# Performance work log

Measured on AMD Instinct MI355X. Metric: run time of the kernel, lower is better.

The kernel has to match this reference:

```python
import jax, jax.numpy as jnp
import numpy as np

N_E = 8192
E_DIM = 256
B = 32768


def setup_inputs() -> dict:
    key = jax.random.key(0)
    kz, ke = jax.random.split(key)
    z = jax.random.normal(kz, (B, E_DIM), dtype=jnp.float32)
    # matches nn.Embedding init: uniform(-1/n_e, 1/n_e)
    embedding = jax.random.uniform(ke, (N_E, E_DIM), dtype=jnp.float32,
                                   minval=-1.0 / N_E, maxval=1.0 / N_E)
    return {"z": z, "embedding": embedding}


def reference(z, embedding):
    # squared euclidean distances: [B, n_e]
    d = (jnp.sum(z * z, axis=1, keepdims=True)
         + jnp.sum(embedding * embedding, axis=1)
         - 2.0 * jnp.einsum('bd,nd->bn', z, embedding))
    min_encoding_indices = jnp.argmin(d, axis=1)          # [B] int
    z_q = embedding[min_encoding_indices]                 # [B, e_dim] gather
    return z_q, min_encoding_indices
```

## Files before the change

### kernel.cpp

```cpp
#include <hip/hip_runtime.h>

constexpr int NE = 8192;
constexpr int ED = 256;
constexpr int BS = 32768;
constexpr float DELTA = 4e-4f;

typedef short bf16x8 __attribute__((ext_vector_type(8)));
typedef float f32x4 __attribute__((ext_vector_type(4)));

constexpr size_t WSTR = (size_t)NE * 64;

__device__ __forceinline__ short f2bf(float f) {
    unsigned u = __float_as_uint(f);
    u = u + 0x7FFFu + ((u >> 16) & 1u);
    return (short)(u >> 16);
}
__device__ __forceinline__ unsigned bf16_rd(float x) {
    unsigned u = __float_as_uint(x);
    unsigned h = u >> 16;
    if ((u & 0x80000000u) && (u & 0xFFFFu)) ++h;
    return h;
}
__device__ __forceinline__ unsigned umn(unsigned a, unsigned b) { return a < b ? a : b; }
__device__ __forceinline__ unsigned umx(unsigned a, unsigned b) { return a > b ? a : b; }

__global__ void sq_np_kernel(const float* __restrict__ a, float* __restrict__ out) {
    int gtid = blockIdx.x * blockDim.x + threadIdx.x;
    int wave = gtid >> 6;
    int lane = threadIdx.x & 63;
    int sub  = lane & 7;
    int row  = wave * 8 + (lane >> 3);
    const float* p = a + (size_t)row * ED;
    float b0 = 0.f, b1 = 0.f;
#pragma unroll
    for (int t = 0; t < 16; ++t) { float v = p[8 * t + sub];       b0 = __fadd_rn(b0, __fmul_rn(v, v)); }
#pragma unroll
    for (int t = 0; t < 16; ++t) { float v = p[128 + 8 * t + sub]; b1 = __fadd_rn(b1, __fmul_rn(v, v)); }
    b0 = __fadd_rn(b0, __shfl_xor(b0, 1));
    b0 = __fadd_rn(b0, __shfl_xor(b0, 2));
    b0 = __fadd_rn(b0, __shfl_xor(b0, 4));
    b1 = __fadd_rn(b1, __shfl_xor(b1, 1));
    b1 = __fadd_rn(b1, __shfl_xor(b1, 2));
    b1 = __fadd_rn(b1, __shfl_xor(b1, 4));
    if (sub == 0) out[row] = __fadd_rn(b0, b1);
}

__global__ void cvt_ebT_kernel(const float* __restrict__ e, char* __restrict__ ebT) {
    int i = blockIdx.x * blockDim.x + threadIdx.x;
    int c = i >> 5;
    int u = i & 31;
    int w = u >> 2, lg = u & 3;
    const float* p = e + (size_t)c * ED + w * 32 + lg * 8;
    float4 v0 = *reinterpret_cast<const float4*>(p);
    float4 v1 = *reinterpret_cast<const float4*>(p + 4);
    bf16x8 h;
    h[0] = f2bf(v0.x); h[1] = f2bf(v0.y); h[2] = f2bf(v0.z); h[3] = f2bf(v0.w);
    h[4] = f2bf(v1.x); h[5] = f2bf(v1.y); h[6] = f2bf(v1.z); h[7] = f2bf(v1.w);
    *reinterpret_cast<bf16x8*>(ebT + (size_t)w * WSTR + (size_t)c * 64 + lg * 16) = h;
}

__global__ void e2slot_kernel(const float* __restrict__ e2, char* __restrict__ ebT) {
    int c = blockIdx.x * blockDim.x + threadIdx.x;
    bf16x8 h = {};
    h[0] = f2bf(e2[c] * -0.5f);
    bf16x8 zz = {};
    char* p = ebT + 8 * WSTR + (size_t)c * 64;
    *reinterpret_cast<bf16x8*>(p)      = h;
    *reinterpret_cast<bf16x8*>(p + 16) = zz;
    *reinterpret_cast<bf16x8*>(p + 32) = zz;
    *reinterpret_cast<bf16x8*>(p + 48) = zz;
}

__device__ __forceinline__ void load_step(bf16x8 (&b)[2][2], const char* abase, int S) {
    int t_ = S >> 3, s_ = S & 7;
    size_t colbyte = (size_t)((t_ << 6) + ((s_ >> 2) << 5)) << 6;
    const char* p = abase + (size_t)((s_ & 3) << 1) * WSTR + colbyte;
    b[0][0] = *reinterpret_cast<const bf16x8*>(p);
    b[0][1] = *reinterpret_cast<const bf16x8*>(p + WSTR);
    b[1][0] = *reinterpret_cast<const bf16x8*>(p + 1024);
    b[1][1] = *reinterpret_cast<const bf16x8*>(p + WSTR + 1024);
}

__global__ __launch_bounds__(256, 2) void vq_pass1(
        const float* __restrict__ z, const char* __restrict__ ebT,
        uint2* __restrict__ wsp) {
    const int tid  = threadIdx.x;
    const int wid  = tid >> 6, lane = tid & 63;
    const int l15  = lane & 15, lg = lane >> 4;
    const int kblk = blockIdx.x;
    const int rg   = (kblk & 7) | ((kblk >> 5) << 3);
    const int q    = (kblk >> 3) & 3;
    const int c0q  = q * 2048;
    const int wr0  = rg * 256 + wid * 64;

    bf16x8 zreg[4][8];
#pragma unroll
    for (int j = 0; j < 4; ++j) {
        const float* zr = z + (size_t)(wr0 + j * 16 + l15) * ED + lg * 8;
#pragma unroll
        for (int t8 = 0; t8 < 8; ++t8) {
            float4 v0 = *reinterpret_cast<const float4*>(zr + t8 * 32);
            float4 v1 = *reinterpret_cast<const float4*>(zr + t8 * 32 + 4);
            bf16x8 h;
            h[0] = f2bf(v0.x); h[1] = f2bf(v0.y); h[2] = f2bf(v0.z); h[3] = f2bf(v0.w);
            h[4] = f2bf(v1.x); h[5] = f2bf(v1.y); h[6] = f2bf(v1.z); h[7] = f2bf(v1.w);
            zreg[j][t8] = h;
        }
    }
    bf16x8 zE = {};
    if (lg == 0) zE[0] = (short)0x3F80;

    const char* abase = ebT + (size_t)(c0q + l15) * 64 + lg * 16;

    bf16x8 buf[2][2][2];
    bf16x8 bufE[2];
    load_step(buf[0], abase, 0);

    unsigned rk1[4], rk2[4];

    for (int t = 0; t < 32; ++t) {
        f32x4 acc[2][4];
#pragma unroll
        for (int s = 0; s < 8; ++s) {
            if ((s & 3) == 0) {
#pragma unroll
                for (int i2 = 0; i2 < 2; ++i2)
#pragma unroll
                    for (int j = 0; j < 4; ++j) acc[i2][j] = (f32x4){0.f, 0.f, 0.f, 0.f};
                size_t colbyte = (size_t)((t << 6) + ((s >> 2) << 5)) << 6;
                bufE[0] = *reinterpret_cast<const bf16x8*>(abase + 8 * WSTR + colbyte);
                bufE[1] = *reinterpret_cast<const bf16x8*>(abase + 8 * WSTR + colbyte + 1024);
            }
            int Sn = t * 8 + s + 1;
            Sn = Sn > 255 ? 255 : Sn;
            load_step(buf[(s + 1) & 1], abase, Sn);
#pragma unroll
            for (int tt = 0; tt < 2; ++tt)
#pragma unroll
                for (int i2 = 0; i2 < 2; ++i2)
#pragma unroll
                    for (int j = 0; j < 4; ++j)
                        acc[i2][j] = __builtin_amdgcn_mfma_f32_16x16x32_bf16(
                            buf[s & 1][i2][tt], zreg[j][(s & 3) * 2 + tt],
                            acc[i2][j], 0, 0, 0);

            if ((s & 3) == 3) {
                const int i0 = (s >> 2) * 2;
#pragma unroll
                for (int i2 = 0; i2 < 2; ++i2)
#pragma unroll
                    for (int j = 0; j < 4; ++j)
                        acc[i2][j] = __builtin_amdgcn_mfma_f32_16x16x32_bf16(
                            bufE[i2], zE, acc[i2][j], 0, 0, 0);

                const unsigned cb = (unsigned)((t & 1) * 64 + lg * 4);
#pragma unroll
                for (int j = 0; j < 4; ++j) {
                    unsigned c1 = 0xFFFFFFFFu, c2 = 0xFFFFFFFFu;
#pragma unroll
                    for (int qp = 0; qp < 2; ++qp) {
                        float va = fmaf(-2.f, acc[0][j][qp * 2],     0.5f);
                        float vb = fmaf(-2.f, acc[0][j][qp * 2 + 1], 0.5f);
                        unsigned ka = (__float_as_uint(va) & 0xFFFFFF80u) | (cb + i0 * 16 + qp * 2);
                        unsigned kb = (__float_as_uint(vb) & 0xFFFFFF80u) | (cb + i0 * 16 + qp * 2 + 1);
                        unsigned lo = umn(ka, kb), hi = umx(ka, kb);
                        unsigned mx = umx(c1, lo);
                        c1 = umn(c1, lo);
                        c2 = umn(umn(c2, hi), mx);
                        va = fmaf(-2.f, acc[1][j][qp * 2],     0.5f);
                        vb = fmaf(-2.f, acc[1][j][qp * 2 + 1], 0.5f);
                        ka = (__float_as_uint(va) & 0xFFFFFF80u) | (cb + (i0 + 1) * 16 + qp * 2);
                        kb = (__float_as_uint(vb) & 0xFFFFFF80u) | (cb + (i0 + 1) * 16 + qp * 2 + 1);
                        lo = umn(ka, kb); hi = umx(ka, kb);
                        mx = umx(c1, lo);
                        c1 = umn(c1, lo);
                        c2 = umn(umn(c2, hi), mx);
                    }
                    if (i0 == 0) {
                        if ((t & 1) == 0) { rk1[j] = c1; rk2[j] = c2; }
                        else {
                            unsigned mxh = umx(rk1[j], c1);
                            rk1[j] = umn(rk1[j], c1);
                            rk2[j] = umn(umn(rk2[j], c2), mxh);
                        }
                    } else {
                        unsigned mxh = umx(rk1[j], c1);
                        c1 = umn(rk1[j], c1);
                        c2 = umn(umn(rk2[j], c2), mxh);
                        if ((t & 1) == 0) {
                            rk1[j] = c1; rk2[j] = c2;
                        } else {
#pragma unroll
                            for (int off = 16; off < 64; off <<= 1) {
                                unsigned o1 = (unsigned)__shfl_xor((int)c1, off);
                                unsigned o2 = (unsigned)__shfl_xor((int)c2, off);
                                unsigned mx2 = umx(c1, o1);
                                c1 = umn(c1, o1);
                                c2 = umn(umn(c2, o2), mx2);
                            }
                            if (lg == 0) {
                                float m1f = __uint_as_float(c1 & 0xFFFFFF80u) - 0.5f;
                                float m2f = __uint_as_float(c2 & 0xFFFFFF80u) - 0.5f;
                                wsp[(size_t)(wr0 + j * 16 + l15) * 64 + (q * 16 + (t >> 1))] =
                                    make_uint2(__float_as_uint(m1f),
                                               (bf16_rd(m2f) << 16) | (c1 & 0x7Fu));
                            }
                        }
                    }
                }
            }
        }
    }
}

__global__ __launch_bounds__(256) void vq_pass2(
        const float* __restrict__ z, const float* __restrict__ e,
        const float* __restrict__ z2, const float* __restrict__ e2,
        const uint2* __restrict__ wsp, float* __restrict__ out) {
    __shared__ __align__(16) float zrow[4][ED];
    const int wid = threadIdx.x >> 6, lane = threadIdx.x & 63;
    const int r = blockIdx.x * 4 + wid;

    *reinterpret_cast<float4*>(&zrow[wid][lane * 4]) =
        *reinterpret_cast<const float4*>(z + (size_t)r * ED + lane * 4);
    __syncthreads();

    const float z2r = z2[r];
    uint2 p = wsp[(size_t)r * 64 + lane];
    float m1 = __uint_as_float(p.x);
    int   i8 = (int)(p.y & 0xFFu);
    float m2 = __uint_as_float(p.y & 0xFFFF0000u);

    float rmn = m1;
#pragma unroll
    for (int off = 1; off < 64; off <<= 1) rmn = fminf(rmn, __shfl_xor(rmn, off));
    const float thr = rmn + DELTA;

    const bool cF = (m2 <= thr);
    const bool cS = (m1 <= thr) && !cF;
    unsigned long long bS = __ballot(cS);
    unsigned long long bF = __ballot(cF);

    float bd = 3.4e38f;
    int   bc = NE;

    int myCol = -1;
    int cnt = 0;
    unsigned long long m = bS;
    while (true) {
        bool flush = (m == 0) || (cnt == 64);
        if (flush) {
            if (cnt > 0) {
                int ecol = (myCol >= 0) ? myCol : 0;
                const float* ec = e + (size_t)ecol * ED;
                float a0 = 0.f, a1 = 0.f, a2 = 0.f, a3 = 0.f;
#pragma unroll 8
                for (int t = 0; t < 64; ++t) {
                    float4 ev = *reinterpret_cast<const float4*>(ec + 4 * t);
                    float4 zv = *reinterpret_cast<const float4*>(&zrow[wid][4 * t]);
                    a0 = __fadd_rn(a0, __fmul_rn(zv.x, ev.x));
                    a1 = __fadd_rn(a1, __fmul_rn(zv.y, ev.y));
                    a2 = __fadd_rn(a2, __fmul_rn(zv.z, ev.z));
                    a3 = __fadd_rn(a3, __fmul_rn(zv.w, ev.w));
                }
                float s = __fadd_rn(__fadd_rn(a0, a1), __fadd_rn(a2, a3));
                float d = __fsub_rn(__fadd_rn(z2r, e2[ecol]), __fmul_rn(2.0f, s));
                if (myCol >= 0 && (d < bd || (d == bd && ecol < bc))) { bd = d; bc = ecol; }
                myCol = -1; cnt = 0;
            }
            if (m == 0) break;
        }
        int ch = __builtin_ctzll(m); m &= m - 1;
        int col = ch * 128 + __shfl(i8, ch);
        if (lane == cnt) myCol = col;
        ++cnt;
    }

    m = bF;
    while (m) {
        int ch = __builtin_ctzll(m); m &= m - 1;
#pragma unroll
        for (int hh = 0; hh < 2; ++hh) {
            int col = ch * 128 + hh * 64 + lane;
            const float* ec = e + (size_t)col * ED;
            float a0 = 0.f, a1 = 0.f, a2 = 0.f, a3 = 0.f;
#pragma unroll 8
            for (int t = 0; t < 64; ++t) {
                float4 ev = *reinterpret_cast<const float4*>(ec + 4 * t);
                float4 zv = *reinterpret_cast<const float4*>(&zrow[wid][4 * t]);
                a0 = __fadd_rn(a0, __fmul_rn(zv.x, ev.x));
                a1 = __fadd_rn(a1, __fmul_rn(zv.y, ev.y));
                a2 = __fadd_rn(a2, __fmul_rn(zv.z, ev.z));
                a3 = __fadd_rn(a3, __fmul_rn(zv.w, ev.w));
            }
            float s = __fadd_rn(__fadd_rn(a0, a1), __fadd_rn(a2, a3));
            float d = __fsub_rn(__fadd_rn(z2r, e2[col]), __fmul_rn(2.0f, s));
            if (d < bd || (d == bd && col < bc)) { bd = d; bc = col; }
        }
    }

#pragma unroll
    for (int off = 1; off < 64; off <<= 1) {
        float od = __shfl_xor(bd, off);
        int   oc = __shfl_xor(bc, off);
        if (od < bd || (od == bd && oc < bc)) { bd = od; bc = oc; }
    }
    if (lane == 0) out[(size_t)BS * ED + r] = (float)bc;
    *reinterpret_cast<float4*>(out + (size_t)r * ED + lane * 4) =
        *reinterpret_cast<const float4*>(e + (size_t)bc * ED + lane * 4);
}

extern "C" void kernel_launch(void* const* d_in, const int* in_sizes, int n_in,
                              void* d_out, int out_size, void* d_ws, size_t ws_size,
                              hipStream_t stream) {
    const float* z = (const float*)d_in[0];
    const float* e = (const float*)d_in[1];
    float* out   = (float*)d_out;
    float* e2np  = (float*)d_ws;
    float* z2np  = e2np + NE;
    uint2* wsp   = (uint2*)(z2np + BS);
    char*  ebT   = (char*)(wsp + (size_t)BS * 64);

    hipLaunchKernelGGL(sq_np_kernel, dim3(NE / 32), dim3(256), 0, stream, e, e2np);
    hipLaunchKernelGGL(sq_np_kernel, dim3(BS / 32), dim3(256), 0, stream, z, z2np);
    hipLaunchKernelGGL(cvt_ebT_kernel, dim3(NE * ED / 8 / 256), dim3(256), 0, stream, e, ebT);
    hipLaunchKernelGGL(e2slot_kernel, dim3(NE / 256), dim3(256), 0, stream, e2np, ebT);
    hipLaunchKernelGGL(vq_pass1, dim3(512), dim3(256), 0, stream, z, ebT, wsp);
    hipLaunchKernelGGL(vq_pass2, dim3(BS / 4), dim3(256), 0, stream, z, e, z2np, e2np, wsp, out);
}
```

Before: 290.1 us.

## Fold -2 scale and bias into MFMA, use med3 top-2, halve rows per wave

Pre-scales the bf16 codebook by -2 and puts e2 plus a constant 0.5 bias into the extra MFMA slot, so accumulators already hold the distance offset and the per-element fma disappears. The top-2 tracking now uses v_med3_u32 instead of min/max chains. Each wave handles 32 rows instead of 64, with twice as many blocks and three blocks per CU, trading fewer registers and more occupancy for more codebook reloads per row. The wave-row mapping and the pass2 workspace layout must stay consistent with the new row grouping.

```diff
diff --git a/kernel.cpp b/kernel.cpp
--- a/kernel.cpp
+++ b/kernel.cpp
@@ -23,6 +23,11 @@
 }
 __device__ __forceinline__ unsigned umn(unsigned a, unsigned b) { return a < b ? a : b; }
 __device__ __forceinline__ unsigned umx(unsigned a, unsigned b) { return a > b ? a : b; }
+__device__ __forceinline__ unsigned med3(unsigned a, unsigned b, unsigned c) {
+    unsigned r;
+    asm("v_med3_u32 %0, %1, %2, %3" : "=v"(r) : "v"(a), "v"(b), "v"(c));
+    return r;
+}
 
 __global__ void sq_np_kernel(const float* __restrict__ a, float* __restrict__ out) {
     int gtid = blockIdx.x * blockDim.x + threadIdx.x;
@@ -54,15 +59,18 @@
     float4 v0 = *reinterpret_cast<const float4*>(p);
     float4 v1 = *reinterpret_cast<const float4*>(p + 4);
     bf16x8 h;
-    h[0] = f2bf(v0.x); h[1] = f2bf(v0.y); h[2] = f2bf(v0.z); h[3] = f2bf(v0.w);
-    h[4] = f2bf(v1.x); h[5] = f2bf(v1.y); h[6] = f2bf(v1.z); h[7] = f2bf(v1.w);
+    h[0] = f2bf(v0.x * -2.f); h[1] = f2bf(v0.y * -2.f);
+    h[2] = f2bf(v0.z * -2.f); h[3] = f2bf(v0.w * -2.f);
+    h[4] = f2bf(v1.x * -2.f); h[5] = f2bf(v1.y * -2.f);
+    h[6] = f2bf(v1.z * -2.f); h[7] = f2bf(v1.w * -2.f);
     *reinterpret_cast<bf16x8*>(ebT + (size_t)w * WSTR + (size_t)c * 64 + lg * 16) = h;
 }
 
 __global__ void e2slot_kernel(const float* __restrict__ e2, char* __restrict__ ebT) {
     int c = blockIdx.x * blockDim.x + threadIdx.x;
     bf16x8 h = {};
-    h[0] = f2bf(e2[c] * -0.5f);
+    h[0] = f2bf(e2[c]);
+    h[1] = f2bf(0.25f);
     bf16x8 zz = {};
     char* p = ebT + 8 * WSTR + (size_t)c * 64;
     *reinterpret_cast<bf16x8*>(p)      = h;
@@ -81,7 +89,7 @@
     b[1][1] = *reinterpret_cast<const bf16x8*>(p + WSTR + 1024);
 }
 
-__global__ __launch_bounds__(256, 2) void vq_pass1(
+__global__ __launch_bounds__(256, 3) void vq_pass1(
         const float* __restrict__ z, const char* __restrict__ ebT,
         uint2* __restrict__ wsp) {
     const int tid  = threadIdx.x;
@@ -91,11 +99,11 @@
     const int rg   = (kblk & 7) | ((kblk >> 5) << 3);
     const int q    = (kblk >> 3) & 3;
     const int c0q  = q * 2048;
-    const int wr0  = rg * 256 + wid * 64;
-
-    bf16x8 zreg[4][8];
-#pragma unroll
-    for (int j = 0; j < 4; ++j) {
+    const int wr0  = rg * 128 + wid * 32;
+
+    bf16x8 zreg[2][8];
+#pragma unroll
+    for (int j = 0; j < 2; ++j) {
         const float* zr = z + (size_t)(wr0 + j * 16 + l15) * ED + lg * 8;
 #pragma unroll
         for (int t8 = 0; t8 < 8; ++t8) {
@@ -108,7 +116,7 @@
         }
     }
     bf16x8 zE = {};
-    if (lg == 0) zE[0] = (short)0x3F80;
+    if (lg == 0) { zE[0] = (short)0x3F80; zE[1] = (short)0x4000; }
 
     const char* abase = ebT + (size_t)(c0q + l15) * 64 + lg * 16;
 
@@ -116,17 +124,17 @@
     bf16x8 bufE[2];
     load_step(buf[0], abase, 0);
 
-    unsigned rk1[4], rk2[4];
+    unsigned rk1[2], rk2[2];
 
     for (int t = 0; t < 32; ++t) {
-        f32x4 acc[2][4];
+        f32x4 acc[2][2];
 #pragma unroll
         for (int s = 0; s < 8; ++s) {
             if ((s & 3) == 0) {
 #pragma unroll
                 for (int i2 = 0; i2 < 2; ++i2)
 #pragma unroll
-                    for (int j = 0; j < 4; ++j) acc[i2][j] = (f32x4){0.f, 0.f, 0.f, 0.f};
+                    for (int j = 0; j < 2; ++j) acc[i2][j] = (f32x4){0.f, 0.f, 0.f, 0.f};
                 size_t colbyte = (size_t)((t << 6) + ((s >> 2) << 5)) << 6;
                 bufE[0] = *reinterpret_cast<const bf16x8*>(abase + 8 * WSTR + colbyte);
                 bufE[1] = *reinterpret_cast<const bf16x8*>(abase + 8 * WSTR + colbyte + 1024);
@@ -139,7 +147,7 @@
 #pragma unroll
                 for (int i2 = 0; i2 < 2; ++i2)
 #pragma unroll
-                    for (int j = 0; j < 4; ++j)
+                    for (int j = 0; j < 2; ++j)
                         acc[i2][j] = __builtin_amdgcn_mfma_f32_16x16x32_bf16(
                             buf[s & 1][i2][tt], zreg[j][(s & 3) * 2 + tt],
                             acc[i2][j], 0, 0, 0);
@@ -149,32 +157,23 @@
 #pragma unroll
                 for (int i2 = 0; i2 < 2; ++i2)
 #pragma unroll
-                    for (int j = 0; j < 4; ++j)
+                    for (int j = 0; j < 2; ++j)
                         acc[i2][j] = __builtin_amdgcn_mfma_f32_16x16x32_bf16(
                             bufE[i2], zE, acc[i2][j], 0, 0, 0);
 
                 const unsigned cb = (unsigned)((t & 1) * 64 + lg * 4);
 #pragma unroll
-                for (int j = 0; j < 4; ++j) {
+                for (int j = 0; j < 2; ++j) {
                     unsigned c1 = 0xFFFFFFFFu, c2 = 0xFFFFFFFFu;
 #pragma unroll
-                    for (int qp = 0; qp < 2; ++qp) {
-                        float va = fmaf(-2.f, acc[0][j][qp * 2],     0.5f);
-                        float vb = fmaf(-2.f, acc[0][j][qp * 2 + 1], 0.5f);
-                        unsigned ka = (__float_as_uint(va) & 0xFFFFFF80u) | (cb + i0 * 16 + qp * 2);
-                        unsigned kb = (__float_as_uint(vb) & 0xFFFFFF80u) | (cb + i0 * 16 + qp * 2 + 1);
-                        unsigned lo = umn(ka, kb), hi = umx(ka, kb);
-                        unsigned mx = umx(c1, lo);
-                        c1 = umn(c1, lo);
-                        c2 = umn(umn(c2, hi), mx);
-                        va = fmaf(-2.f, acc[1][j][qp * 2],     0.5f);
-                        vb = fmaf(-2.f, acc[1][j][qp * 2 + 1], 0.5f);
-                        ka = (__float_as_uint(va) & 0xFFFFFF80u) | (cb + (i0 + 1) * 16 + qp * 2);
-                        kb = (__float_as_uint(vb) & 0xFFFFFF80u) | (cb + (i0 + 1) * 16 + qp * 2 + 1);
-                        lo = umn(ka, kb); hi = umx(ka, kb);
-                        mx = umx(c1, lo);
-                        c1 = umn(c1, lo);
-                        c2 = umn(umn(c2, hi), mx);
+                    for (int i2 = 0; i2 < 2; ++i2) {
+#pragma unroll
+                        for (int qq = 0; qq < 4; ++qq) {
+                            unsigned k = (__float_as_uint(acc[i2][j][qq]) & 0xFFFFFF80u)
+                                       | (cb + (i0 + i2) * 16 + qq);
+                            c2 = med3(c1, c2, k);
+                            c1 = umn(c1, k);
+                        }
                     }
                     if (i0 == 0) {
                         if ((t & 1) == 0) { rk1[j] = c1; rk2[j] = c2; }
@@ -325,6 +324,6 @@
     hipLaunchKernelGGL(sq_np_kernel, dim3(BS / 32), dim3(256), 0, stream, z, z2np);
     hipLaunchKernelGGL(cvt_ebT_kernel, dim3(NE * ED / 8 / 256), dim3(256), 0, stream, e, ebT);
     hipLaunchKernelGGL(e2slot_kernel, dim3(NE / 256), dim3(256), 0, stream, e2np, ebT);
-    hipLaunchKernelGGL(vq_pass1, dim3(512), dim3(256), 0, stream, z, ebT, wsp);
+    hipLaunchKernelGGL(vq_pass1, dim3(1024), dim3(256), 0, stream, z, ebT, wsp);
     hipLaunchKernelGGL(vq_pass2, dim3(BS / 4), dim3(256), 0, stream, z, e, z2np, e2np, wsp, out);
 }
```

Measured after the change: 401.6 us. 1.38x slower.
